# Performance work log

Measured on AMD Instinct MI355X. Metric: run time of the kernel, lower is better.

## Reference

```python
import jax, jax.numpy as jnp
import numpy as np

N_EXC = 1024
N_INH = 256
BATCH = 2048
TAU_E = 10.0
TAU_I = 5.0
DT = 0.1
STEPS = 10


def _ring_weights(sigma, n_exc):
    # Fixed ring topology: Gaussian in wrapped angular distance, row-normalized, zero diagonal.
    angles = jnp.linspace(0.0, 2.0 * jnp.pi, n_exc, dtype=jnp.float32)
    d = angles[None, :] - angles[:, None]                  # [n_exc, n_exc]
    d = jnp.arctan2(jnp.sin(d), jnp.cos(d))                # wrap to (-pi, pi]
    W = jnp.exp(-0.5 * (d / sigma) ** 2)
    W = W / W.sum(axis=1, keepdims=True)
    W = W * (1.0 - jnp.eye(n_exc, dtype=W.dtype))          # fill_diagonal_(0)
    return W


def setup_inputs() -> dict:
    key = jax.random.key(0)
    k_ext, k_h, k_ei, k_ie = jax.random.split(key, 4)
    return {
        "external_input": jax.random.normal(k_ext, (BATCH, N_EXC), dtype=jnp.float32),
        "h": jax.random.uniform(k_h, (BATCH, N_EXC), dtype=jnp.float32),
        "sigma_ee": jnp.float32(0.5),
        "W_EI": jax.random.normal(k_ei, (N_EXC, N_INH), dtype=jnp.float32) * 0.1,
        "W_IE": jax.random.normal(k_ie, (N_INH, N_EXC), dtype=jnp.float32) * 0.1,
        "g_ee": jnp.float32(1.0),
        "g_ei": jnp.float32(1.5),
        "g_ie": jnp.float32(2.0),
        "g_input": jnp.float32(1.0),
        "noise_rate_e": jnp.float32(0.1),
        "noise_rate_i": jnp.float32(0.05),
        "steps": STEPS,
    }


def reference(external_input, h, sigma_ee, W_EI, W_IE, g_ee, g_ei, g_ie, g_input,
              noise_rate_e, noise_rate_i, steps):
    B, n_exc = external_input.shape
    n_inh = W_EI.shape[1]
    # sigma_ee is constant across steps -> compute the ring weights once (same math).
    W_EE = _ring_weights(sigma_ee, n_exc)
    r_e0 = h                                               # eval path with h provided
    r_i0 = jnp.zeros((B, n_inh), dtype=h.dtype)
    noise_key = jax.random.key(42)

    def step(carry, t):
        r_e, r_i = carry
        ke, ki = jax.random.split(jax.random.fold_in(noise_key, t))
        # batched versions of the per-sample matmuls
        input_e = (g_ee * jnp.einsum('ij,bj->bi', W_EE, r_e)
                   - g_ie * jnp.einsum('bj,ji->bi', r_i, W_IE)
                   + g_input * external_input)
        input_i = g_ei * jnp.einsum('be,ei->bi', r_e, W_EI)
        # Poisson noise, mean-subtracted (torch.poisson is non-differentiable).
        pe = jax.lax.stop_gradient(
            jax.random.poisson(ke, jax.lax.stop_gradient(noise_rate_e), input_e.shape)
        ).astype(input_e.dtype)
        pi = jax.lax.stop_gradient(
            jax.random.poisson(ki, jax.lax.stop_gradient(noise_rate_i), input_i.shape)
        ).astype(input_i.dtype)
        input_e = input_e + (pe - noise_rate_e)
        input_i = input_i + (pi - noise_rate_i)
        r_e = jax.nn.relu(r_e + DT * (-r_e + jax.nn.relu(input_e)) / TAU_E)
        r_i = jax.nn.relu(r_i + DT * (-r_i + jax.nn.relu(input_i)) / TAU_I)
        return (r_e, r_i), None

    (r_e, r_i), _ = jax.lax.scan(step, (r_e0, r_i0), jnp.arange(steps))
    return r_e
```

## Files before the change

kernel.cpp:

```cpp
#include <hip/hip_runtime.h>
#include <cstdint>


#define N_EXC 1024
#define N_INH 256
#define BATCH 2048
#define STEPS 10
#define MAX_POIS 32
#define NE_TOT (BATCH * N_EXC)
#define NTOT   (NE_TOT + BATCH * N_INH)
#define NZ_SLICES 8

typedef short s16x8 __attribute__((ext_vector_type(8)));
typedef float f32x4 __attribute__((ext_vector_type(4)));

typedef __attribute__((address_space(1))) const void GV;
typedef __attribute__((address_space(3))) void LV;

struct U2 { uint32_t x, y; };

__device__ __forceinline__ uint32_t rotl32(uint32_t v, int r) {
  return (v << r) | (v >> (32 - r));
}

__device__ __forceinline__ U2 threefry(U2 k, uint32_t x0, uint32_t x1) {
  uint32_t ks0 = k.x, ks1 = k.y, ks2 = k.x ^ k.y ^ 0x1BD11BDAu;
  x0 += ks0; x1 += ks1;
#define TF_R4(a,b,c,d) \
  x0 += x1; x1 = rotl32(x1,a); x1 ^= x0; \
  x0 += x1; x1 = rotl32(x1,b); x1 ^= x0; \
  x0 += x1; x1 = rotl32(x1,c); x1 ^= x0; \
  x0 += x1; x1 = rotl32(x1,d); x1 ^= x0;
  TF_R4(13,15,26,6)  x0 += ks1; x1 += ks2 + 1u;
  TF_R4(17,29,16,24) x0 += ks2; x1 += ks0 + 2u;
  TF_R4(13,15,26,6)  x0 += ks0; x1 += ks1 + 3u;
  TF_R4(17,29,16,24) x0 += ks1; x1 += ks2 + 4u;
  TF_R4(13,15,26,6)  x0 += ks2; x1 += ks0 + 5u;
#undef TF_R4
  U2 r; r.x = x0; r.y = x1; return r;
}

__device__ __forceinline__ unsigned short f2b(float f) {
  uint32_t u = __float_as_uint(f);
  return (unsigned short)((u + 0x7FFFu + ((u >> 16) & 1u)) >> 16);
}

__device__ __forceinline__ void gload16(const void* g, void* l) {
  __builtin_amdgcn_global_load_lds((GV*)g, (LV*)l, 16, 0, 0);
}

__device__ void gen_noise(int f0, int stride,
                          const U2* __restrict__ ske, const U2* __restrict__ ski,
                          float lam_e, float lam_i,
                          uint8_t* __restrict__ nze, uint8_t* __restrict__ nzi) {
  for (int f = f0; f < NTOT; f += stride) {
    bool ii = f >= NE_TOT;
    uint32_t e = ii ? (uint32_t)(f - NE_TOT) : (uint32_t)f;
    const U2* sk = ii ? ski : ske;
    float neg = ii ? -lam_i : -lam_e;
    float lp = 0.0f;
    int k = 0;
#pragma unroll 1
    for (int n = 0; n < MAX_POIS; ++n) {
      if (!(lp > neg)) break;
      k++;
      U2 h = threefry(sk[n], 0u, e);
      uint32_t bits = h.x ^ h.y;
      float u = __uint_as_float((bits >> 9) | 0x3f800000u) - 1.0f;
      lp += logf(u);
    }
    (ii ? nzi : nze)[e] = (uint8_t)(k - 1);
  }
}

__global__ void keys_kernel(U2* subk_e, U2* subk_i) {
  int tid = threadIdx.x;
  if (tid >= 2 * STEPS) return;
  int t = tid >> 1;
  bool is_i = tid & 1;
  U2 base; base.x = 0u; base.y = 42u;
  U2 folded = threefry(base, 0u, (uint32_t)t);
  U2 ke = threefry(folded, 0u, 0u);
  U2 ki = threefry(folded, 0u, 1u);
  U2 rng = is_i ? ki : ke;
  U2* dst = (is_i ? subk_i : subk_e) + t * MAX_POIS;
  for (int n = 0; n < MAX_POIS; ++n) {
    dst[n] = threefry(rng, 0u, 1u);
    rng = threefry(rng, 0u, 0u);
  }
}

__global__ __launch_bounds__(256) void noise0_kernel(
    const U2* __restrict__ subk_e, const U2* __restrict__ subk_i,
    const float* __restrict__ sc_rate_e, const float* __restrict__ sc_rate_i,
    uint8_t* __restrict__ nze, uint8_t* __restrict__ nzi) {
  int flat = blockIdx.x * 256 + threadIdx.x;
  gen_noise(flat, gridDim.x * 256, subk_e, subk_i, *sc_rate_e, *sc_rate_i, nze, nzi);
}

__global__ __launch_bounds__(256) void wee_kernel(const float* __restrict__ sigma_p,
                                                  unsigned short* __restrict__ W) {
  int i = blockIdx.x;
  int tid = threadIdx.x;
  float sigma = *sigma_p;
  const float twopi = 6.28318530717958647692f;
  const float delta = twopi / 1023.0f;
  float ai = (float)i * delta;
  float w[4];
  float s = 0.0f;
#pragma unroll
  for (int q = 0; q < 4; ++q) {
    int j = tid + q * 256;
    float aj = (float)j * delta;
    float d = aj - ai;
    float wd = atan2f(sinf(d), cosf(d));
    float x = wd / sigma;
    float v = expf(-0.5f * x * x);
    w[q] = v;
    s += v;
  }
  __shared__ float red[256];
  red[tid] = s;
  __syncthreads();
  for (int off = 128; off > 0; off >>= 1) {
    if (tid < off) red[tid] += red[tid + off];
    __syncthreads();
  }
  float sum = red[0];
#pragma unroll
  for (int q = 0; q < 4; ++q) {
    int j = tid + q * 256;
    W[i * N_EXC + j] = (j == i) ? (unsigned short)0 : f2b(w[q] / sum);
  }
}

__global__ void setup_kernel(const float* __restrict__ W_EI, const float* __restrict__ W_IE,
                             const float* __restrict__ h,
                             unsigned short* __restrict__ W_EIT,
                             unsigned short* __restrict__ W_IET,
                             unsigned short* __restrict__ hb) {
  int tid = blockIdx.x * blockDim.x + threadIdx.x;
  int nt = gridDim.x * blockDim.x;
  for (int i = tid; i < BATCH * N_EXC; i += nt) hb[i] = f2b(h[i]);
  for (int i = tid; i < N_INH * N_EXC; i += nt) {
    int r = i >> 10, c = i & 1023;
    W_EIT[i] = f2b(W_EI[c * N_INH + r]);
  }
  for (int i = tid; i < N_EXC * N_INH; i += nt) {
    int r = i >> 8, c = i & 255;
    W_IET[i] = f2b(W_IE[c * N_EXC + r]);
  }
}

#define PIPE_GEMM(APTR, LDA, AROW0, BPTR, LDB, BROW0, KLEN, ACC)                \
  {                                                                             \
    const int NT = (KLEN) / 64;                                                 \
    int c0 = wave * 128 + lane;                                                 \
    int c1 = c0 + 64;                                                           \
    int r0 = c0 >> 3, q0 = ((c0 & 7) ^ (r0 & 7)) << 3;                          \
    int r1 = c1 >> 3, q1 = ((c1 & 7) ^ (r1 & 7)) << 3;                          \
    const unsigned short* ap0 = (APTR) + (size_t)((AROW0) + r0) * (LDA) + q0;   \
    const unsigned short* ap1 = (APTR) + (size_t)((AROW0) + r1) * (LDA) + q1;   \
    const unsigned short* bp0 = (BPTR) + (size_t)((BROW0) + r0) * (LDB) + q0;   \
    const unsigned short* bp1 = (BPTR) + (size_t)((BROW0) + r1) * (LDB) + q1;   \
    char* la0 = (char*)As + wave * 2048;                                        \
    char* la1 = la0 + 1024;                                                     \
    char* lb0 = (char*)Bs + wave * 2048;                                        \
    char* lb1 = lb0 + 1024;                                                     \
    gload16(ap0, la0); gload16(ap1, la1);                                       \
    gload16(bp0, lb0); gload16(bp1, lb1);                                       \
    int cur = 0;                                                                \
    int raf0 = wr * 32 + l16, raf1 = raf0 + 16;                                 \
    int rbf0 = wc * 32 + l16, rbf1 = rbf0 + 16;                                 \
    int aA0 = (raf0 << 7) | ((lhi ^ (raf0 & 7)) << 4);                          \
    int aA1 = (raf1 << 7) | ((lhi ^ (raf1 & 7)) << 4);                          \
    int aB0 = (rbf0 << 7) | ((lhi ^ (rbf0 & 7)) << 4);                          \
    int aB1 = (rbf1 << 7) | ((lhi ^ (rbf1 & 7)) << 4);                          \
    for (int kt = 0; kt < NT; ++kt) {                                           \
      __syncthreads();                                                          \
      if (kt + 1 < NT) {                                                        \
        int k0 = (kt + 1) * 64;                                                 \
        int nb = (cur ^ 1) * 8192;                                              \
        gload16(ap0 + k0, la0 + nb); gload16(ap1 + k0, la1 + nb);               \
        gload16(bp0 + k0, lb0 + nb); gload16(bp1 + k0, lb1 + nb);               \
      }                                                                         \
      const char* ab = (const char*)As + cur * 8192;                            \
      const char* bb = (const char*)Bs + cur * 8192;                            \
      _Pragma("unroll")                                                         \
      for (int ks = 0; ks < 2; ++ks) {                                          \
        int kx = ks << 6;                                                       \
        s16x8 af0 = *(const s16x8*)(ab + (aA0 ^ kx));                           \
        s16x8 af1 = *(const s16x8*)(ab + (aA1 ^ kx));                           \
        s16x8 bf0 = *(const s16x8*)(bb + (aB0 ^ kx));                           \
        s16x8 bf1 = *(const s16x8*)(bb + (aB1 ^ kx));                           \
        ACC[0][0] = __builtin_amdgcn_mfma_f32_16x16x32_bf16(af0, bf0, ACC[0][0], 0, 0, 0); \
        ACC[0][1] = __builtin_amdgcn_mfma_f32_16x16x32_bf16(af0, bf1, ACC[0][1], 0, 0, 0); \
        ACC[1][0] = __builtin_amdgcn_mfma_f32_16x16x32_bf16(af1, bf0, ACC[1][0], 0, 0, 0); \
        ACC[1][1] = __builtin_amdgcn_mfma_f32_16x16x32_bf16(af1, bf1, ACC[1][1], 0, 0, 0); \
      }                                                                         \
      cur ^= 1;                                                                 \
    }                                                                           \
  }

__global__ __launch_bounds__(256) void step_kernel(
    const float* __restrict__ re_in, const unsigned short* __restrict__ reb_in,
    const float* __restrict__ ri_in, const unsigned short* __restrict__ rib_in,
    const unsigned short* __restrict__ W_EEb, const unsigned short* __restrict__ W_IET,
    const unsigned short* __restrict__ W_EIT,
    const float* __restrict__ ext,
    const float* __restrict__ sc_gee, const float* __restrict__ sc_gei,
    const float* __restrict__ sc_gie, const float* __restrict__ sc_gin,
    const float* __restrict__ sc_rate_e, const float* __restrict__ sc_rate_i,
    const uint8_t* __restrict__ nz_e_in, const uint8_t* __restrict__ nz_i_in,
    uint8_t* __restrict__ nz_e_out, uint8_t* __restrict__ nz_i_out,
    const U2* __restrict__ subk_e_next, const U2* __restrict__ subk_i_next,
    float* __restrict__ re_out, unsigned short* __restrict__ reb_out,
    float* __restrict__ ri_out, unsigned short* __restrict__ rib_out) {
  __shared__ __align__(16) short As[2 * 4096];
  __shared__ __align__(16) short Bs[2 * 4096];
  int tid = threadIdx.x;

  if (blockIdx.y >= 20) {
    if (nz_e_out != nullptr) {
      int flat = ((blockIdx.y - 20) * gridDim.x + blockIdx.x) * 256 + tid;
      gen_noise(flat, NZ_SLICES * 32 * 256, subk_e_next, subk_i_next,
                *sc_rate_e, *sc_rate_i, nz_e_out, nz_i_out);
    }
    return;
  }

  int lane = tid & 63;
  int wave = tid >> 6;
  int wr = wave >> 1, wc = wave & 1;
  int l16 = lane & 15, lhi = lane >> 4;
  int b0 = blockIdx.x * 64;
  bool is_e = blockIdx.y < 16;
  int i0 = (is_e ? blockIdx.y : (blockIdx.y - 16)) * 64;

  f32x4 acc[2][2] = {};
  f32x4 acc2[2][2] = {};

  if (is_e) {
    PIPE_GEMM(reb_in, N_EXC, b0, W_EEb, N_EXC, i0, N_EXC, acc);
    if (rib_in != nullptr) {
      PIPE_GEMM(rib_in, N_INH, b0, W_IET, N_INH, i0, N_INH, acc2);
    }
    float gee = *sc_gee, gie = *sc_gie, gin = *sc_gin, rate = *sc_rate_e;
#pragma unroll
    for (int mm = 0; mm < 2; ++mm)
#pragma unroll
      for (int nn = 0; nn < 2; ++nn)
#pragma unroll
        for (int q = 0; q < 4; ++q) {
          int row = b0 + wr * 32 + mm * 16 + lhi * 4 + q;
          int col = i0 + wc * 32 + nn * 16 + l16;
          int idx = row * N_EXC + col;
          float val = gee * acc[mm][nn][q] - gie * acc2[mm][nn][q] + gin * ext[idx];
          val += (float)nz_e_in[idx] - rate;
          float ro = re_in[idx];
          float rn = ro + (0.1f * (fmaxf(val, 0.0f) - ro)) / 10.0f;
          rn = fmaxf(rn, 0.0f);
          re_out[idx] = rn;
          reb_out[idx] = f2b(rn);
        }
  } else {
    PIPE_GEMM(reb_in, N_EXC, b0, W_EIT, N_EXC, i0, N_EXC, acc);
    float gei = *sc_gei, rate = *sc_rate_i;
#pragma unroll
    for (int mm = 0; mm < 2; ++mm)
#pragma unroll
      for (int nn = 0; nn < 2; ++nn)
#pragma unroll
        for (int q = 0; q < 4; ++q) {
          int row = b0 + wr * 32 + mm * 16 + lhi * 4 + q;
          int col = i0 + wc * 32 + nn * 16 + l16;
          int idx = row * N_INH + col;
          float val = gei * acc[mm][nn][q];
          val += (float)nz_i_in[idx] - rate;
          float rio = (ri_in != nullptr) ? ri_in[idx] : 0.0f;
          float rn = rio + (0.1f * (fmaxf(val, 0.0f) - rio)) / 5.0f;
          rn = fmaxf(rn, 0.0f);
          ri_out[idx] = rn;
          rib_out[idx] = f2b(rn);
        }
  }
}

extern "C" void kernel_launch(void* const* d_in, const int* in_sizes, int n_in,
                              void* d_out, int out_size, void* d_ws, size_t ws_size,
                              hipStream_t stream) {
  const float* ext    = (const float*)d_in[0];
  const float* h      = (const float*)d_in[1];
  const float* sigma  = (const float*)d_in[2];
  const float* W_EI   = (const float*)d_in[3];
  const float* W_IE   = (const float*)d_in[4];
  const float* g_ee   = (const float*)d_in[5];
  const float* g_ei   = (const float*)d_in[6];
  const float* g_ie   = (const float*)d_in[7];
  const float* g_in   = (const float*)d_in[8];
  const float* rate_e = (const float*)d_in[9];
  const float* rate_i = (const float*)d_in[10];

  char* ws = (char*)d_ws;
  unsigned short* W_EEb = (unsigned short*)ws; ws += (size_t)N_EXC * N_EXC * 2;
  unsigned short* W_EIT = (unsigned short*)ws; ws += (size_t)N_INH * N_EXC * 2;
  unsigned short* W_IET = (unsigned short*)ws; ws += (size_t)N_EXC * N_INH * 2;
  float* reA            = (float*)ws;          ws += (size_t)BATCH * N_EXC * 4;
  unsigned short* rebA  = (unsigned short*)ws; ws += (size_t)BATCH * N_EXC * 2;
  unsigned short* rebB  = (unsigned short*)ws; ws += (size_t)BATCH * N_EXC * 2;
  float* riA            = (float*)ws;          ws += (size_t)BATCH * N_INH * 4;
  float* riB            = (float*)ws;          ws += (size_t)BATCH * N_INH * 4;
  unsigned short* ribA  = (unsigned short*)ws; ws += (size_t)BATCH * N_INH * 2;
  unsigned short* ribB  = (unsigned short*)ws; ws += (size_t)BATCH * N_INH * 2;
  uint8_t* nzE0         = (uint8_t*)ws;        ws += (size_t)NE_TOT;
  uint8_t* nzE1         = (uint8_t*)ws;        ws += (size_t)NE_TOT;
  uint8_t* nzI0         = (uint8_t*)ws;        ws += (size_t)BATCH * N_INH;
  uint8_t* nzI1         = (uint8_t*)ws;        ws += (size_t)BATCH * N_INH;
  U2* subk_e            = (U2*)ws;             ws += (size_t)(STEPS + 1) * MAX_POIS * sizeof(U2);
  U2* subk_i            = (U2*)ws;             ws += (size_t)(STEPS + 1) * MAX_POIS * sizeof(U2);
  float* re_dout = (float*)d_out;

  wee_kernel<<<dim3(N_EXC), dim3(256), 0, stream>>>(sigma, W_EEb);
  setup_kernel<<<dim3(512), dim3(256), 0, stream>>>(W_EI, W_IE, h, W_EIT, W_IET, rebB);
  keys_kernel<<<dim3(1), dim3(64), 0, stream>>>(subk_e, subk_i);
  noise0_kernel<<<dim3(512), dim3(256), 0, stream>>>(subk_e, subk_i, rate_e, rate_i,
                                                     nzE0, nzI0);

  for (int t = 0; t < STEPS; ++t) {
    const float* re_in          = (t == 0) ? h : ((t & 1) ? reA : re_dout);
    float* re_out               = (t & 1) ? re_dout : reA;
    const unsigned short* rb_in = (t & 1) ? rebA : rebB;
    unsigned short* rb_out      = (t & 1) ? rebB : rebA;
    const float* ri_in          = (t == 0) ? nullptr : ((t & 1) ? riA : riB);
    float* ri_out               = (t & 1) ? riB : riA;
    const unsigned short* ib_in = (t == 0) ? nullptr : ((t & 1) ? ribA : ribB);
    unsigned short* ib_out      = (t & 1) ? ribB : ribA;
    const uint8_t* nze_in       = (t & 1) ? nzE1 : nzE0;
    const uint8_t* nzi_in       = (t & 1) ? nzI1 : nzI0;
    uint8_t* nze_out            = (t + 1 < STEPS) ? ((t & 1) ? nzE0 : nzE1) : nullptr;
    uint8_t* nzi_out            = (t + 1 < STEPS) ? ((t & 1) ? nzI0 : nzI1) : nullptr;

    step_kernel<<<dim3(BATCH / 64, 20 + NZ_SLICES), dim3(256), 0, stream>>>(
        re_in, rb_in, ri_in, ib_in, W_EEb, W_IET, W_EIT, ext,
        g_ee, g_ei, g_ie, g_in, rate_e, rate_i,
        nze_in, nzi_in, nze_out, nzi_out,
        subk_e + (t + 1) * MAX_POIS, subk_i + (t + 1) * MAX_POIS,
        re_out, rb_out, ri_out, ib_out);
  }
}
```

Before: 443.9 us.

## Enlarge GEMM block tile to 128x64 with 2x4 MFMA fragments per wave

The batch dimension of each block's tile doubles from 64 to 128 rows. Each wave now owns 32 rows by all 64 columns, computing 2x4 MFMA fragments, so every B fragment loaded from LDS is reused across more work and each weight tile is fetched once per 128 batch rows instead of 64. The grid halves in x, and NZ_SLICES doubles so the noise-generation blocks still cover the same number of elements. The cost is more LDS (48 KB), more accumulator registers, and fewer GEMM blocks, which can lower occupancy and SM fill.

```diff
diff --git a/kernel.cpp b/kernel.cpp
--- a/kernel.cpp
+++ b/kernel.cpp
@@ -9,7 +9,7 @@
 #define MAX_POIS 32
 #define NE_TOT (BATCH * N_EXC)
 #define NTOT   (NE_TOT + BATCH * N_INH)
-#define NZ_SLICES 8
+#define NZ_SLICES 16
 
 typedef short s16x8 __attribute__((ext_vector_type(8)));
 typedef float f32x4 __attribute__((ext_vector_type(4)));
@@ -155,48 +155,58 @@
 #define PIPE_GEMM(APTR, LDA, AROW0, BPTR, LDB, BROW0, KLEN, ACC)                \
   {                                                                             \
     const int NT = (KLEN) / 64;                                                 \
-    int c0 = wave * 128 + lane;                                                 \
-    int c1 = c0 + 64;                                                           \
-    int r0 = c0 >> 3, q0 = ((c0 & 7) ^ (r0 & 7)) << 3;                          \
-    int r1 = c1 >> 3, q1 = ((c1 & 7) ^ (r1 & 7)) << 3;                          \
-    const unsigned short* ap0 = (APTR) + (size_t)((AROW0) + r0) * (LDA) + q0;   \
-    const unsigned short* ap1 = (APTR) + (size_t)((AROW0) + r1) * (LDA) + q1;   \
-    const unsigned short* bp0 = (BPTR) + (size_t)((BROW0) + r0) * (LDB) + q0;   \
-    const unsigned short* bp1 = (BPTR) + (size_t)((BROW0) + r1) * (LDB) + q1;   \
-    char* la0 = (char*)As + wave * 2048;                                        \
-    char* la1 = la0 + 1024;                                                     \
-    char* lb0 = (char*)Bs + wave * 2048;                                        \
-    char* lb1 = lb0 + 1024;                                                     \
-    gload16(ap0, la0); gload16(ap1, la1);                                       \
-    gload16(bp0, lb0); gload16(bp1, lb1);                                       \
+    int ja[4], jb[2];                                                           \
+    _Pragma("unroll") for (int p = 0; p < 4; ++p) ja[p] = p * 256 + tid;        \
+    _Pragma("unroll") for (int p = 0; p < 2; ++p) jb[p] = p * 256 + tid;        \
+    const unsigned short* apg[4];                                               \
+    const unsigned short* bpg[2];                                               \
+    _Pragma("unroll") for (int p = 0; p < 4; ++p) {                             \
+      int r = ja[p] >> 3, c8 = (ja[p] & 7) ^ (r & 7);                           \
+      apg[p] = (APTR) + (size_t)((AROW0) + r) * (LDA) + c8 * 8;                 \
+    }                                                                           \
+    _Pragma("unroll") for (int p = 0; p < 2; ++p) {                             \
+      int r = jb[p] >> 3, c8 = (jb[p] & 7) ^ (r & 7);                           \
+      bpg[p] = (BPTR) + (size_t)((BROW0) + r) * (LDB) + c8 * 8;                 \
+    }                                                                           \
+    char* lA[4]; char* lB[2];                                                   \
+    _Pragma("unroll") for (int p = 0; p < 4; ++p)                               \
+      lA[p] = (char*)As + p * 4096 + wave * 1024;                               \
+    _Pragma("unroll") for (int p = 0; p < 2; ++p)                               \
+      lB[p] = (char*)Bs + p * 4096 + wave * 1024;                               \
+    _Pragma("unroll") for (int p = 0; p < 4; ++p) gload16(apg[p], lA[p]);       \
+    _Pragma("unroll") for (int p = 0; p < 2; ++p) gload16(bpg[p], lB[p]);       \
     int cur = 0;                                                                \
-    int raf0 = wr * 32 + l16, raf1 = raf0 + 16;                                 \
-    int rbf0 = wc * 32 + l16, rbf1 = rbf0 + 16;                                 \
-    int aA0 = (raf0 << 7) | ((lhi ^ (raf0 & 7)) << 4);                          \
-    int aA1 = (raf1 << 7) | ((lhi ^ (raf1 & 7)) << 4);                          \
-    int aB0 = (rbf0 << 7) | ((lhi ^ (rbf0 & 7)) << 4);                          \
-    int aB1 = (rbf1 << 7) | ((lhi ^ (rbf1 & 7)) << 4);                          \
+    int ra0 = wave * 32 + l16, ra1 = ra0 + 16;                                  \
+    int aA0 = (ra0 << 7) | ((lhi ^ (ra0 & 7)) << 4);                            \
+    int aA1 = (ra1 << 7) | ((lhi ^ (ra1 & 7)) << 4);                            \
+    int aB[4];                                                                  \
+    _Pragma("unroll") for (int n = 0; n < 4; ++n) {                             \
+      int rb = n * 16 + l16;                                                    \
+      aB[n] = (rb << 7) | ((lhi ^ (rb & 7)) << 4);                              \
+    }                                                                           \
     for (int kt = 0; kt < NT; ++kt) {                                           \
       __syncthreads();                                                          \
       if (kt + 1 < NT) {                                                        \
         int k0 = (kt + 1) * 64;                                                 \
-        int nb = (cur ^ 1) * 8192;                                              \
-        gload16(ap0 + k0, la0 + nb); gload16(ap1 + k0, la1 + nb);               \
-        gload16(bp0 + k0, lb0 + nb); gload16(bp1 + k0, lb1 + nb);               \
+        int nbA = (cur ^ 1) * 16384, nbB = (cur ^ 1) * 8192;                    \
+        _Pragma("unroll") for (int p = 0; p < 4; ++p)                           \
+          gload16(apg[p] + k0, lA[p] + nbA);                                    \
+        _Pragma("unroll") for (int p = 0; p < 2; ++p)                           \
+          gload16(bpg[p] + k0, lB[p] + nbB);                                    \
       }                                                                         \
-      const char* ab = (const char*)As + cur * 8192;                            \
+      const char* ab = (const char*)As + cur * 16384;                           \
       const char* bb = (const char*)Bs + cur * 8192;                            \
       _Pragma("unroll")                                                         \
       for (int ks = 0; ks < 2; ++ks) {                                          \
         int kx = ks << 6;                                                       \
         s16x8 af0 = *(const s16x8*)(ab + (aA0 ^ kx));                           \
         s16x8 af1 = *(const s16x8*)(ab + (aA1 ^ kx));                           \
-        s16x8 bf0 = *(const s16x8*)(bb + (aB0 ^ kx));                           \
-        s16x8 bf1 = *(const s16x8*)(bb + (aB1 ^ kx));                           \
-        ACC[0][0] = __builtin_amdgcn_mfma_f32_16x16x32_bf16(af0, bf0, ACC[0][0], 0, 0, 0); \
-        ACC[0][1] = __builtin_amdgcn_mfma_f32_16x16x32_bf16(af0, bf1, ACC[0][1], 0, 0, 0); \
-        ACC[1][0] = __builtin_amdgcn_mfma_f32_16x16x32_bf16(af1, bf0, ACC[1][0], 0, 0, 0); \
-        ACC[1][1] = __builtin_amdgcn_mfma_f32_16x16x32_bf16(af1, bf1, ACC[1][1], 0, 0, 0); \
+        _Pragma("unroll")                                                       \
+        for (int n = 0; n < 4; ++n) {                                           \
+          s16x8 bf = *(const s16x8*)(bb + (aB[n] ^ kx));                        \
+          ACC[0][n] = __builtin_amdgcn_mfma_f32_16x16x32_bf16(af0, bf, ACC[0][n], 0, 0, 0); \
+          ACC[1][n] = __builtin_amdgcn_mfma_f32_16x16x32_bf16(af1, bf, ACC[1][n], 0, 0, 0); \
+        }                                                                       \
       }                                                                         \
       cur ^= 1;                                                                 \
     }                                                                           \
@@ -216,14 +226,14 @@
     const U2* __restrict__ subk_e_next, const U2* __restrict__ subk_i_next,
     float* __restrict__ re_out, unsigned short* __restrict__ reb_out,
     float* __restrict__ ri_out, unsigned short* __restrict__ rib_out) {
-  __shared__ __align__(16) short As[2 * 4096];
+  __shared__ __align__(16) short As[2 * 8192];
   __shared__ __align__(16) short Bs[2 * 4096];
   int tid = threadIdx.x;
 
   if (blockIdx.y >= 20) {
     if (nz_e_out != nullptr) {
       int flat = ((blockIdx.y - 20) * gridDim.x + blockIdx.x) * 256 + tid;
-      gen_noise(flat, NZ_SLICES * 32 * 256, subk_e_next, subk_i_next,
+      gen_noise(flat, NZ_SLICES * 16 * 256, subk_e_next, subk_i_next,
                 *sc_rate_e, *sc_rate_i, nz_e_out, nz_i_out);
     }
     return;
@@ -231,14 +241,13 @@
 
   int lane = tid & 63;
   int wave = tid >> 6;
-  int wr = wave >> 1, wc = wave & 1;
   int l16 = lane & 15, lhi = lane >> 4;
-  int b0 = blockIdx.x * 64;
+  int b0 = blockIdx.x * 128;
   bool is_e = blockIdx.y < 16;
   int i0 = (is_e ? blockIdx.y : (blockIdx.y - 16)) * 64;
 
-  f32x4 acc[2][2] = {};
-  f32x4 acc2[2][2] = {};
+  f32x4 acc[2][4] = {};
+  f32x4 acc2[2][4] = {};
 
   if (is_e) {
     PIPE_GEMM(reb_in, N_EXC, b0, W_EEb, N_EXC, i0, N_EXC, acc);
@@ -249,11 +258,11 @@
 #pragma unroll
     for (int mm = 0; mm < 2; ++mm)
 #pragma unroll
-      for (int nn = 0; nn < 2; ++nn)
+      for (int nn = 0; nn < 4; ++nn)
 #pragma unroll
         for (int q = 0; q < 4; ++q) {
-          int row = b0 + wr * 32 + mm * 16 + lhi * 4 + q;
-          int col = i0 + wc * 32 + nn * 16 + l16;
+          int row = b0 + wave * 32 + mm * 16 + lhi * 4 + q;
+          int col = i0 + nn * 16 + l16;
           int idx = row * N_EXC + col;
           float val = gee * acc[mm][nn][q] - gie * acc2[mm][nn][q] + gin * ext[idx];
           val += (float)nz_e_in[idx] - rate;
@@ -269,11 +278,11 @@
 #pragma unroll
     for (int mm = 0; mm < 2; ++mm)
 #pragma unroll
-      for (int nn = 0; nn < 2; ++nn)
+      for (int nn = 0; nn < 4; ++nn)
 #pragma unroll
         for (int q = 0; q < 4; ++q) {
-          int row = b0 + wr * 32 + mm * 16 + lhi * 4 + q;
-          int col = i0 + wc * 32 + nn * 16 + l16;
+          int row = b0 + wave * 32 + mm * 16 + lhi * 4 + q;
+          int col = i0 + nn * 16 + l16;
           int idx = row * N_INH + col;
           float val = gei * acc[mm][nn][q];
           val += (float)nz_i_in[idx] - rate;
@@ -340,7 +349,7 @@
     uint8_t* nze_out            = (t + 1 < STEPS) ? ((t & 1) ? nzE0 : nzE1) : nullptr;
     uint8_t* nzi_out            = (t + 1 < STEPS) ? ((t & 1) ? nzI0 : nzI1) : nullptr;
 
-    step_kernel<<<dim3(BATCH / 64, 20 + NZ_SLICES), dim3(256), 0, stream>>>(
+    step_kernel<<<dim3(BATCH / 128, 20 + NZ_SLICES), dim3(256), 0, stream>>>(
         re_in, rb_in, ri_in, ib_in, W_EEb, W_IET, W_EIT, ext,
         g_ee, g_ei, g_ie, g_in, rate_e, rate_i,
         nze_in, nzi_in, nze_out, nzi_out,
```

New measurement: 454.4 us. 2.4% more time.
